# Performance work log

Hardware: AMD Instinct MI355X
Metric: run time of the kernel (lower is better)

## Reference

```python
import jax, jax.numpy as jnp
import numpy as np

DIM = 1024
D_STATE = 16
D_CONV = 4
EXPAND = 2
D_INNER = EXPAND * DIM          # 2048
DT_RANK = (DIM + 15) // 16      # 64 (mamba_ssm 'auto')
B_SZ = 2
SEQ = 1024


def setup_inputs() -> dict:
    key = jax.random.key(0)
    ks = jax.random.split(key, 10)
    s = 0.02
    x = jax.random.normal(ks[0], (B_SZ, SEQ, DIM), jnp.float32)
    mask = jnp.ones((B_SZ, SEQ), dtype=bool)
    in_proj_w = jax.random.normal(ks[1], (DIM, 2 * D_INNER), jnp.float32) * s
    conv_w = jax.random.normal(ks[2], (D_INNER, D_CONV), jnp.float32) * 0.2
    conv_b = jnp.zeros((D_INNER,), jnp.float32)
    x_proj_w = jax.random.normal(ks[3], (D_INNER, DT_RANK + 2 * D_STATE), jnp.float32) * s
    dt_proj_w = jax.random.normal(ks[4], (DT_RANK, D_INNER), jnp.float32) * (DT_RANK ** -0.5)
    # inverse-softplus-style small positive dt bias, like mamba_ssm init
    dt = jnp.exp(jax.random.uniform(ks[5], (D_INNER,)) * (np.log(0.1) - np.log(0.001)) + np.log(0.001))
    dt_proj_b = dt + jnp.log(-jnp.expm1(-dt))
    # A_log init: log(1..d_state) per channel (S4D-real init)
    A_log = jnp.log(jnp.tile(jnp.arange(1, D_STATE + 1, dtype=jnp.float32)[None, :], (D_INNER, 1)))
    D = jnp.ones((D_INNER,), jnp.float32)
    out_proj_w = jax.random.normal(ks[6], (D_INNER, DIM), jnp.float32) * s
    return {"x": x, "mask": mask, "in_proj_w": in_proj_w, "conv_w": conv_w,
            "conv_b": conv_b, "x_proj_w": x_proj_w, "dt_proj_w": dt_proj_w,
            "dt_proj_b": dt_proj_b, "A_log": A_log, "D": D, "out_proj_w": out_proj_w}


def _mamba(x, in_proj_w, conv_w, conv_b, x_proj_w, dt_proj_w, dt_proj_b, A_log, D, out_proj_w):
    B, L, _ = x.shape
    xz = x @ in_proj_w                       # (B, L, 2*d_inner)
    xc, z = jnp.split(xz, 2, axis=-1)
    # causal depthwise conv1d (padding=d_conv-1, truncated to L)
    xp = jnp.pad(xc, ((0, 0), (D_CONV - 1, 0), (0, 0)))
    conv = conv_b
    for k in range(D_CONV):
        conv = conv + xp[:, k:k + L, :] * conv_w[:, k]
    u = jax.nn.silu(conv)                    # (B, L, d_inner)
    x_dbl = u @ x_proj_w                     # (B, L, dt_rank + 2*d_state)
    dtr, Bm, Cm = jnp.split(x_dbl, [DT_RANK, DT_RANK + D_STATE], axis=-1)
    delta = jax.nn.softplus(dtr @ dt_proj_w + dt_proj_b)   # (B, L, d_inner)
    A = -jnp.exp(A_log)                      # (d_inner, d_state)
    dA = jnp.exp(jnp.einsum('bld,dn->bldn', delta, A))     # (B, L, d_inner, d_state)
    dBu = jnp.einsum('bld,bln->bldn', delta * u, Bm)

    def step(h, inp):
        dA_t, dBu_t, C_t = inp
        h = dA_t * h + dBu_t                 # (B, d_inner, d_state)
        y = jnp.einsum('bdn,bn->bd', h, C_t)
        return h, y

    h0 = jnp.zeros((B, D_INNER, D_STATE), x.dtype)
    _, ys = jax.lax.scan(step, h0, (dA.transpose(1, 0, 2, 3),
                                    dBu.transpose(1, 0, 2, 3),
                                    Cm.transpose(1, 0, 2)))
    y = ys.transpose(1, 0, 2) + u * D        # (B, L, d_inner)
    y = y * jax.nn.silu(z)
    return y @ out_proj_w                    # (B, L, dim)


def reference(x, mask, in_proj_w, conv_w, conv_b, x_proj_w, dt_proj_w, dt_proj_b, A_log, D, out_proj_w):
    out = _mamba(x, in_proj_w, conv_w, conv_b, x_proj_w, dt_proj_w, dt_proj_b, A_log, D, out_proj_w)
    # dropout=0.0 -> Identity; masked_fill(~mask, 0)
    return jnp.where(mask[:, :, None], out, 0.0)
```

## Files before the change

kernel.cpp:

```cpp
#include <hip/hip_runtime.h>
#include <hip/hip_bf16.h>

#define DIMX 1024
#define DSTATE 16
#define DCONV 4
#define DINNER 2048
#define DTRANK 64
#define BSZ 2
#define SEQL 1024
#define NROW (BSZ*SEQL)
#define NPROJ (DTRANK + 2*DSTATE)
#define NCH2 32
#define CL2 32
#define G2SPLIT 16
#define G2KLEN (DINNER / G2SPLIT)
#define G4SPLIT 2

typedef __bf16 bf16x8 __attribute__((ext_vector_type(8)));
typedef float f32x4 __attribute__((ext_vector_type(4)));
typedef unsigned short ushort8_t __attribute__((ext_vector_type(8)));

#define LOG2E 1.44269504088896340736f

__device__ __forceinline__ float sigmoidf_(float x){ return 1.0f/(1.0f+__expf(-x)); }
__device__ __forceinline__ float fexp2(float x){ return __builtin_amdgcn_exp2f(x); }
__device__ __forceinline__ unsigned short f2bf(float f){
  union { float f; unsigned int i; } c; c.f = f;
  unsigned int r = (c.i + 0x7FFFu + ((c.i >> 16) & 1u)) >> 16;
  return (unsigned short)r;
}
__device__ __forceinline__ float bf2f(unsigned short u){
  union { unsigned int i; float f; } c; c.i = ((unsigned int)u) << 16; return c.f;
}

__device__ __forceinline__ void gload16(const void* g, void* l){
  __builtin_amdgcn_global_load_lds(
      (const __attribute__((address_space(1))) unsigned int*)g,
      (__attribute__((address_space(3))) unsigned int*)l, 16, 0, 0);
}

__global__ __launch_bounds__(256) void prep_k(
    const float* __restrict__ x, unsigned short* __restrict__ xb,
    const float* __restrict__ w1, unsigned short* __restrict__ w1t,
    const float* __restrict__ w4, unsigned short* __restrict__ w4t,
    const float* __restrict__ dtw, unsigned short* __restrict__ dtwt,
    const float* __restrict__ xpw, unsigned short* __restrict__ xpwt)
{
  __shared__ unsigned short T[32][33];
  int blk = blockIdx.x;
  if (blk < 2048) {
    const int i = blk*256 + threadIdx.x;
    float4 v = *(const float4*)(x + (size_t)i * 4);
    ushort4 o;
    o.x = f2bf(v.x); o.y = f2bf(v.y); o.z = f2bf(v.z); o.w = f2bf(v.w);
    *(ushort4*)(xb + (size_t)i * 4) = o;
    return;
  }
  blk -= 2048;
  if (blk >= 6464) {
    blk -= 6464;
    const int i = blk*256 + threadIdx.x;
    *(ushort4*)(xpwt + (size_t)96*DINNER + (size_t)i*4) = make_ushort4(0,0,0,0);
    return;
  }
  const float* w; unsigned short* wt; int K, N, nT, kT;
  if (blk < 4096) {
    w = w1; wt = w1t; K = 1024; N = 4096;
    nT = (blk & 127) * 32; kT = (blk >> 7) * 32;
  } else if (blk < 6144) {
    blk -= 4096;
    w = w4; wt = w4t; K = 2048; N = 1024;
    nT = (blk & 31) * 32; kT = (blk >> 5) * 32;
  } else if (blk < 6272) {
    blk -= 6144;
    w = dtw; wt = dtwt; K = 64; N = 2048;
    nT = (blk & 63) * 32; kT = (blk >> 6) * 32;
  } else {
    blk -= 6272;
    w = xpw; wt = xpwt; K = 2048; N = 96;
    nT = (blk % 3) * 32; kT = (blk / 3) * 32;
  }
  const int tx = threadIdx.x & 31, ty = threadIdx.x >> 5;
  #pragma unroll
  for (int i = 0; i < 4; i++)
    T[tx][ty + i*8] = f2bf(w[(size_t)(kT + ty + i*8) * N + nT + tx]);
  __syncthreads();
  #pragma unroll
  for (int i = 0; i < 4; i++)
    wt[(size_t)(nT + ty + i*8) * K + kT + tx] = T[ty + i*8][tx];
}

__global__ __launch_bounds__(256) void gemm1_bf2_k(
    const unsigned short* __restrict__ A, int lda,
    const unsigned short* __restrict__ BT, int ldb,
    unsigned short* __restrict__ X0, unsigned short* __restrict__ X1,
    int splitN, int ldc, int K)
{
  constexpr int BM = 128, BN = 128, BK = 32, NB = 4;
  __shared__ unsigned short As[NB][BM*BK];
  __shared__ unsigned short Bs[NB][BN*BK];

  const int tid = threadIdx.x;
  const int w = tid >> 6, lane = tid & 63;
  const int quad = lane >> 4, lrow = lane & 15;
  const int mOff = (w & 1) * 64, nOff = (w >> 1) * 64;
  const int rowTile = blockIdx.y * BM, colTile = blockIdx.x * BN;

  f32x4 acc[4][4] = {};

  const int srow = lane >> 2;
  const int sbyte = (lane & 3) * 16;

  for (int k0 = 0; k0 < K; k0 += NB*BK) {
    #pragma unroll
    for (int hh = 0; hh < NB; hh++) {
      const int kk = k0 + hh*BK;
      const char* aSrc = (const char*)(A  + (size_t)(rowTile + w*32 + srow)*lda + kk) + sbyte;
      const char* bSrc = (const char*)(BT + (size_t)(colTile + w*32 + srow)*ldb + kk) + sbyte;
      gload16(aSrc,                    &As[hh][(w*32     )*32]);
      gload16(aSrc + 16*(size_t)lda*2, &As[hh][(w*32 + 16)*32]);
      gload16(bSrc,                    &Bs[hh][(w*32     )*32]);
      gload16(bSrc + 16*(size_t)ldb*2, &Bs[hh][(w*32 + 16)*32]);
    }
    __syncthreads();

    #pragma unroll
    for (int hh = 0; hh < NB; hh++) {
      bf16x8 af[4], bfr[4];
      #pragma unroll
      for (int mi = 0; mi < 4; mi++)
        af[mi] = *(const bf16x8*)&As[hh][(mOff + mi*16 + lrow)*32 + quad*8];
      #pragma unroll
      for (int ni = 0; ni < 4; ni++)
        bfr[ni] = *(const bf16x8*)&Bs[hh][(nOff + ni*16 + lrow)*32 + quad*8];
      #pragma unroll
      for (int mi = 0; mi < 4; mi++)
        #pragma unroll
        for (int ni = 0; ni < 4; ni++)
          acc[mi][ni] = __builtin_amdgcn_mfma_f32_16x16x32_bf16(
              af[mi], bfr[ni], acc[mi][ni], 0, 0, 0);
    }
    __syncthreads();
  }

  unsigned short* Cb = (colTile < splitN) ? X0 : X1;
  const int cBase = (colTile < splitN) ? colTile : colTile - splitN;

  #pragma unroll
  for (int mi = 0; mi < 4; mi++) {
    #pragma unroll
    for (int ni = 0; ni < 4; ni++) {
      const int row = rowTile + mOff + mi*16 + quad*4;
      const int cc = cBase + nOff + ni*16 + lrow;
      #pragma unroll
      for (int r = 0; r < 4; r++)
        Cb[(size_t)(row + r) * ldc + cc] = f2bf(acc[mi][ni][r]);
    }
  }
}

__global__ __launch_bounds__(256) void gemm2_k(
    const unsigned short* __restrict__ A,
    const unsigned short* __restrict__ BT,
    float* __restrict__ g2p)
{
  constexpr int BM = 64, BK = 32;
  __shared__ unsigned short As[2][BM*BK];
  __shared__ unsigned short Bs[2][128*BK];

  const int tid = threadIdx.x;
  const int w = tid >> 6, lane = tid & 63;
  const int quad = lane >> 4, lrow = lane & 15;
  const int mOff = (w & 1) * 32, nOff = (w >> 1) * 64;
  const int rowTile = blockIdx.x * BM;
  const int kBeg = blockIdx.y * G2KLEN;

  f32x4 acc[2][4] = {};

  const int srow = lane >> 2;
  const int sbyte = (lane & 3) * 16;

  for (int k0 = kBeg; k0 < kBeg + G2KLEN; k0 += 2*BK) {
    #pragma unroll
    for (int hh = 0; hh < 2; hh++) {
      const int kk = k0 + hh*BK;
      const char* aSrc = (const char*)(A  + (size_t)(rowTile + w*16 + srow)*DINNER + kk) + sbyte;
      const char* bSrc = (const char*)(BT + (size_t)(w*32 + srow)*DINNER + kk) + sbyte;
      gload16(aSrc,                       &As[hh][(w*16     )*32]);
      gload16(bSrc,                       &Bs[hh][(w*32     )*32]);
      gload16(bSrc + 16*(size_t)DINNER*2, &Bs[hh][(w*32 + 16)*32]);
    }
    __syncthreads();

    #pragma unroll
    for (int hh = 0; hh < 2; hh++) {
      bf16x8 af[2], bfr[4];
      #pragma unroll
      for (int mi = 0; mi < 2; mi++)
        af[mi] = *(const bf16x8*)&As[hh][(mOff + mi*16 + lrow)*32 + quad*8];
      #pragma unroll
      for (int ni = 0; ni < 4; ni++)
        bfr[ni] = *(const bf16x8*)&Bs[hh][(nOff + ni*16 + lrow)*32 + quad*8];
      #pragma unroll
      for (int mi = 0; mi < 2; mi++)
        #pragma unroll
        for (int ni = 0; ni < 4; ni++)
          acc[mi][ni] = __builtin_amdgcn_mfma_f32_16x16x32_bf16(
              af[mi], bfr[ni], acc[mi][ni], 0, 0, 0);
    }
    __syncthreads();
  }

  float* P = g2p + (size_t)blockIdx.y * NROW * NPROJ;
  #pragma unroll
  for (int mi = 0; mi < 2; mi++) {
    #pragma unroll
    for (int ni = 0; ni < 4; ni++) {
      const int row = rowTile + mOff + mi*16 + quad*4;
      const int col = nOff + ni*16 + lrow;
      if (col >= NPROJ) continue;
      #pragma unroll
      for (int r = 0; r < 4; r++)
        P[(size_t)(row + r) * NPROJ + col] = acc[mi][ni][r];
    }
  }
}

__global__ __launch_bounds__(256) void reduce_xdbl_k(
    const float* __restrict__ g2p, float* __restrict__ xdbl)
{
  const int i = blockIdx.x * 256 + threadIdx.x;
  f32x4 v = *(const f32x4*)(g2p + (size_t)i * 4);
  #pragma unroll
  for (int s = 1; s < G2SPLIT; s++)
    v += *(const f32x4*)(g2p + (size_t)s * NROW * NPROJ + (size_t)i * 4);
  *(f32x4*)(xdbl + (size_t)i * 4) = v;
}

__global__ __launch_bounds__(256) void gemm4_k(
    const unsigned short* __restrict__ A,
    const unsigned short* __restrict__ BT,
    float* __restrict__ g4p)
{
  constexpr int BM = 64, BN = 128, BK = 32, NB = 4;
  constexpr int KCH = DINNER / G4SPLIT;
  __shared__ unsigned short As[NB][BM*BK];
  __shared__ unsigned short Bs[NB][BN*BK];

  const int tid = threadIdx.x;
  const int w = tid >> 6, lane = tid & 63;
  const int quad = lane >> 4, lrow = lane & 15;
  const int mOff = (w & 1) * 32, nOff = (w >> 1) * 64;
  const int rowTile = blockIdx.y * BM, colTile = blockIdx.x * BN;
  const int kBeg = blockIdx.z * KCH;

  f32x4 acc[2][4] = {};

  const int srow = lane >> 2;
  const int sbyte = (lane & 3) * 16;

  for (int k0 = kBeg; k0 < kBeg + KCH; k0 += NB*BK) {
    #pragma unroll
    for (int hh = 0; hh < NB; hh++) {
      const int kk = k0 + hh*BK;
      const char* aSrc = (const char*)(A  + (size_t)(rowTile + w*16 + srow)*DINNER + kk) + sbyte;
      const char* bSrc = (const char*)(BT + (size_t)(colTile + w*32 + srow)*DINNER + kk) + sbyte;
      gload16(aSrc,                       &As[hh][(w*16     )*32]);
      gload16(bSrc,                       &Bs[hh][(w*32     )*32]);
      gload16(bSrc + 16*(size_t)DINNER*2, &Bs[hh][(w*32 + 16)*32]);
    }
    __syncthreads();

    #pragma unroll
    for (int hh = 0; hh < NB; hh++) {
      bf16x8 af[2], bfr[4];
      #pragma unroll
      for (int mi = 0; mi < 2; mi++)
        af[mi] = *(const bf16x8*)&As[hh][(mOff + mi*16 + lrow)*32 + quad*8];
      #pragma unroll
      for (int ni = 0; ni < 4; ni++)
        bfr[ni] = *(const bf16x8*)&Bs[hh][(nOff + ni*16 + lrow)*32 + quad*8];
      #pragma unroll
      for (int mi = 0; mi < 2; mi++)
        #pragma unroll
        for (int ni = 0; ni < 4; ni++)
          acc[mi][ni] = __builtin_amdgcn_mfma_f32_16x16x32_bf16(
              af[mi], bfr[ni], acc[mi][ni], 0, 0, 0);
    }
    __syncthreads();
  }

  float* P = g4p + (size_t)blockIdx.z * NROW * DIMX;
  #pragma unroll
  for (int mi = 0; mi < 2; mi++) {
    #pragma unroll
    for (int ni = 0; ni < 4; ni++) {
      const int row = rowTile + mOff + mi*16 + quad*4;
      const int col = colTile + nOff + ni*16 + lrow;
      #pragma unroll
      for (int r = 0; r < 4; r++)
        P[(size_t)(row + r) * DIMX + col] = acc[mi][ni][r];
    }
  }
}

__global__ __launch_bounds__(256) void reduce_out_k(
    const float* __restrict__ g4p, float* __restrict__ outp)
{
  const int i = blockIdx.x * 256 + threadIdx.x;
  f32x4 v = *(const f32x4*)(g4p + (size_t)i * 4);
  #pragma unroll
  for (int s = 1; s < G4SPLIT; s++)
    v += *(const f32x4*)(g4p + (size_t)s * NROW * DIMX + (size_t)i * 4);
  *(f32x4*)(outp + (size_t)i * 4) = v;
}

__global__ __launch_bounds__(256) void gemm3_k(
    const float* __restrict__ xdbl,
    const unsigned short* __restrict__ dtwt,
    const float* __restrict__ bias,
    unsigned short* __restrict__ delta16)
{
  __shared__ float As[64][68];
  __shared__ float Bs[64][68];
  const int tid = threadIdx.x;
  const int tx = tid & 15, ty = tid >> 4;
  const int rowTile = blockIdx.y * 64;
  const int colTile = blockIdx.x * 64;

  const int ar = tid >> 2;
  const int ak = (tid & 3) * 4;

  #pragma unroll
  for (int kc = 0; kc < 4; kc++) {
    const int kk = kc*16 + ak;
    float4 av = *(const float4*)(xdbl + (size_t)(rowTile + ar) * NPROJ + kk);
    As[kk+0][ar] = av.x; As[kk+1][ar] = av.y;
    As[kk+2][ar] = av.z; As[kk+3][ar] = av.w;
    ushort4 bv = *(const ushort4*)(dtwt + (size_t)(colTile + ar) * DTRANK + kk);
    Bs[kk+0][ar] = bf2f(bv.x); Bs[kk+1][ar] = bf2f(bv.y);
    Bs[kk+2][ar] = bf2f(bv.z); Bs[kk+3][ar] = bf2f(bv.w);
  }
  __syncthreads();

  float acc[4][4] = {};
  #pragma unroll 8
  for (int k = 0; k < DTRANK; k++) {
    float4 a4 = *(const float4*)&As[k][ty*4];
    float4 b4 = *(const float4*)&Bs[k][tx*4];
    float a[4] = {a4.x, a4.y, a4.z, a4.w};
    float b[4] = {b4.x, b4.y, b4.z, b4.w};
    #pragma unroll
    for (int i = 0; i < 4; i++)
      #pragma unroll
      for (int j = 0; j < 4; j++)
        acc[i][j] += a[i] * b[j];
  }

  float4 bb = *(const float4*)(bias + colTile + tx*4);
  const float bvv[4] = {bb.x, bb.y, bb.z, bb.w};
  #pragma unroll
  for (int i = 0; i < 4; i++) {
    const int r = rowTile + ty*4 + i;
    ushort4 o;
    float vv[4];
    #pragma unroll
    for (int j = 0; j < 4; j++) {
      float v = acc[i][j] + bvv[j];
      vv[j] = (v > 20.f) ? v : log1pf(__expf(v));
    }
    o.x = f2bf(vv[0]); o.y = f2bf(vv[1]); o.z = f2bf(vv[2]); o.w = f2bf(vv[3]);
    *(ushort4*)(delta16 + (size_t)r * DINNER + colTile + tx*4) = o;
  }
}

__global__ __launch_bounds__(256) void conv_silu_k(
    const unsigned short* __restrict__ xcb,
    const float* __restrict__ conv_w,
    const float* __restrict__ conv_b,
    unsigned short* __restrict__ ub)
{
  const int idx = blockIdx.x * 256 + threadIdx.x;
  const int d4 = (idx & (DINNER/4 - 1)) * 4;
  const int row = idx >> 9;
  const int l = row & (SEQL - 1);

  float4 cb = *(const float4*)(conv_b + d4);
  float acc[4] = {cb.x, cb.y, cb.z, cb.w};
  float4 w0 = *(const float4*)(conv_w + (size_t)(d4+0)*4);
  float4 w1 = *(const float4*)(conv_w + (size_t)(d4+1)*4);
  float4 w2 = *(const float4*)(conv_w + (size_t)(d4+2)*4);
  float4 w3 = *(const float4*)(conv_w + (size_t)(d4+3)*4);
  const float* wp[4] = {(const float*)&w0, (const float*)&w1,
                        (const float*)&w2, (const float*)&w3};
  #pragma unroll
  for (int k = 0; k < DCONV; k++) {
    const int ls = l + k - (DCONV - 1);
    if (ls >= 0) {
      ushort4 xv = *(const ushort4*)(xcb + (size_t)(row + k - (DCONV - 1)) * DINNER + d4);
      acc[0] += bf2f(xv.x) * wp[0][k];
      acc[1] += bf2f(xv.y) * wp[1][k];
      acc[2] += bf2f(xv.z) * wp[2][k];
      acc[3] += bf2f(xv.w) * wp[3][k];
    }
  }
  ushort4 o;
  o.x = f2bf(acc[0] * sigmoidf_(acc[0]));
  o.y = f2bf(acc[1] * sigmoidf_(acc[1]));
  o.z = f2bf(acc[2] * sigmoidf_(acc[2]));
  o.w = f2bf(acc[3] * sigmoidf_(acc[3]));
  *(ushort4*)(ub + (size_t)row * DINNER + d4) = o;
}

__global__ __launch_bounds__(256) void scan_a(
    const unsigned short* __restrict__ delta16,
    const unsigned short* __restrict__ ub,
    const float* __restrict__ xdbl,
    const float* __restrict__ A_log,
    float* __restrict__ S, float* __restrict__ sumd_g)
{
  const int bx = blockIdx.x;
  const int c  = bx & (NCH2-1);
  const int dg = (bx / NCH2) & 7;
  const int b  = bx / (NCH2*8);
  const int d = dg * 256 + threadIdx.x;
  const size_t row0 = (size_t)(b*SEQL + c*CL2);

  __shared__ float bc_s[CL2][32];
  {
    const int t = threadIdx.x >> 3;
    const int cc = (threadIdx.x & 7) * 4;
    *(float4*)&bc_s[t][cc] = *(const float4*)&xdbl[(row0 + t)*NPROJ + DTRANK + cc];
  }

  float A2[16];
  #pragma unroll
  for (int i = 0; i < 4; i++) {
    float4 al = *(const float4*)&A_log[(size_t)d*DSTATE + i*4];
    A2[i*4+0] = -__expf(al.x)*LOG2E; A2[i*4+1] = -__expf(al.y)*LOG2E;
    A2[i*4+2] = -__expf(al.z)*LOG2E; A2[i*4+3] = -__expf(al.w)*LOG2E;
  }

  float dlt[CL2], uu[CL2];
  #pragma unroll
  for (int t = 0; t < CL2; t++) {
    dlt[t] = bf2f(delta16[(row0 + t)*DINNER + d]);
    uu[t]  = bf2f(ub[(row0 + t)*DINNER + d]);
  }
  __syncthreads();

  float h[16];
  #pragma unroll
  for (int n = 0; n < 16; n++) h[n] = 0.f;
  float sd = 0.f;

  #pragma unroll
  for (int t = 0; t < CL2; t++) {
    const float du = dlt[t] * uu[t];
    sd += dlt[t];
    f32x4 bq[4];
    #pragma unroll
    for (int i = 0; i < 4; i++) bq[i] = *(const f32x4*)&bc_s[t][i*4];
    #pragma unroll
    for (int n = 0; n < 16; n++) {
      const float a = fexp2(dlt[t] * A2[n]);
      h[n] = a * h[n] + du * bq[n>>2][n&3];
    }
  }

  const size_t base = ((size_t)(b*NCH2 + c) * DINNER + d) * DSTATE;
  #pragma unroll
  for (int i = 0; i < 4; i++) {
    f32x4 hv; hv[0]=h[i*4+0]; hv[1]=h[i*4+1]; hv[2]=h[i*4+2]; hv[3]=h[i*4+3];
    *(f32x4*)&S[base + i*4] = hv;
  }
  sumd_g[(size_t)(b*NCH2 + c) * DINNER + d] = sd;
}

__global__ __launch_bounds__(256) void scan_b(
    const float* __restrict__ S, const float* __restrict__ sumd_g,
    const float* __restrict__ A_log, float* __restrict__ H)
{
  const int idx = blockIdx.x * 256 + threadIdx.x;
  const int n = idx & 15, d = (idx >> 4) & (DINNER-1), b = idx >> 15;
  const float A2 = -__expf(A_log[(size_t)d*DSTATE + n]) * LOG2E;
  float h = 0.f;
  size_t pos = ((size_t)(b*NCH2) * DINNER + d) * DSTATE + n;
  size_t sp  = (size_t)(b*NCH2) * DINNER + d;
  const size_t pstep = (size_t)DINNER * DSTATE;
  #pragma unroll 4
  for (int c = 0; c < NCH2; c++) {
    const float sd = sumd_g[sp];
    const float Sv = S[pos];
    H[pos] = h;
    h = fexp2(A2 * sd) * h + Sv;
    pos += pstep; sp += DINNER;
  }
}

__global__ __launch_bounds__(256) void scan_c(
    const unsigned short* __restrict__ delta16,
    const unsigned short* __restrict__ ub,
    const unsigned short* __restrict__ zb,
    const float* __restrict__ xdbl,
    const float* __restrict__ A_log,
    const float* __restrict__ Dp,
    const float* __restrict__ H,
    unsigned short* __restrict__ Y)
{
  const int bx = blockIdx.x;
  const int c  = bx & (NCH2-1);
  const int dg = (bx / NCH2) & 7;
  const int b  = bx / (NCH2*8);
  const int d = dg * 256 + threadIdx.x;
  const size_t row0 = (size_t)(b*SEQL + c*CL2);

  __shared__ float bc_s[CL2][32];
  {
    const int t = threadIdx.x >> 3;
    const int cc = (threadIdx.x & 7) * 4;
    *(float4*)&bc_s[t][cc] = *(const float4*)&xdbl[(row0 + t)*NPROJ + DTRANK + cc];
  }

  float A2[16];
  #pragma unroll
  for (int i = 0; i < 4; i++) {
    float4 al = *(const float4*)&A_log[(size_t)d*DSTATE + i*4];
    A2[i*4+0] = -__expf(al.x)*LOG2E; A2[i*4+1] = -__expf(al.y)*LOG2E;
    A2[i*4+2] = -__expf(al.z)*LOG2E; A2[i*4+3] = -__expf(al.w)*LOG2E;
  }
  const float Dval = Dp[d];

  float dlt[CL2], uu[CL2], zz[CL2];
  #pragma unroll
  for (int t = 0; t < CL2; t++) {
    dlt[t] = bf2f(delta16[(row0 + t)*DINNER + d]);
    uu[t]  = bf2f(ub[(row0 + t)*DINNER + d]);
    zz[t]  = bf2f(zb[(row0 + t)*DINNER + d]);
  }

  float h[16];
  {
    const size_t hb = ((size_t)(b*NCH2 + c) * DINNER + d) * DSTATE;
    #pragma unroll
    for (int i = 0; i < 4; i++) {
      f32x4 hv = *(const f32x4*)&H[hb + i*4];
      h[i*4+0]=hv[0]; h[i*4+1]=hv[1]; h[i*4+2]=hv[2]; h[i*4+3]=hv[3];
    }
  }
  __syncthreads();

  #pragma unroll
  for (int t = 0; t < CL2; t++) {
    const float du = dlt[t] * uu[t];
    f32x4 bq[4], cq[4];
    #pragma unroll
    for (int i = 0; i < 4; i++) {
      bq[i] = *(const f32x4*)&bc_s[t][i*4];
      cq[i] = *(const f32x4*)&bc_s[t][16 + i*4];
    }
    float y = 0.f;
    #pragma unroll
    for (int n = 0; n < 16; n++) {
      const float a = fexp2(dlt[t] * A2[n]);
      h[n] = a * h[n] + du * bq[n>>2][n&3];
      y += h[n] * cq[n>>2][n&3];
    }
    const float yy = (y + uu[t]*Dval) * (zz[t] * sigmoidf_(zz[t]));
    Y[(row0 + t)*DINNER + d] = f2bf(yy);
  }
}

extern "C" void kernel_launch(void* const* d_in, const int* in_sizes, int n_in,
                              void* d_out, int out_size, void* d_ws, size_t ws_size,
                              hipStream_t stream) {
  const float* x         = (const float*)d_in[0];
  const float* in_proj_w = (const float*)d_in[2];
  const float* conv_w    = (const float*)d_in[3];
  const float* conv_b    = (const float*)d_in[4];
  const float* x_proj_w  = (const float*)d_in[5];
  const float* dt_proj_w = (const float*)d_in[6];
  const float* dt_proj_b = (const float*)d_in[7];
  const float* A_log     = (const float*)d_in[8];
  const float* Dp        = (const float*)d_in[9];
  const float* out_proj_w= (const float*)d_in[10];
  float* out = (float*)d_out;

  char* B = (char*)d_ws;
  unsigned short* xcb  = (unsigned short*)B;
  unsigned short* yb   = (unsigned short*)B;
  float* xdbl = (float*)(B + (34ll<<20));
  unsigned short* delta16 = (unsigned short*)(B + (35ll<<20));
  unsigned short* w1t  = (unsigned short*)(B + (44ll<<20));
  unsigned short* w4t  = (unsigned short*)(B + (53ll<<20));
  unsigned short* dtwt = (unsigned short*)(B + (58ll<<20));
  unsigned short* xb   = (unsigned short*)(B + (59ll<<20));
  unsigned short* xpwt = (unsigned short*)(B + (64ll<<20));
  float* S2   = (float*)(B + (72ll<<20));
  float* H2   = (float*)(B + (90ll<<20));
  float* sumd = (float*)(B + (108ll<<20));
  unsigned short* zb = (unsigned short*)(B + (110ll<<20));
  unsigned short* ub = (unsigned short*)(B + (119ll<<20));
  float* g4p  = (float*)(B + (136ll<<20));
  float* g2p  = (float*)(B + (172ll<<20));

  dim3 blk(256);

  prep_k<<<dim3(2048 + 4096 + 2048 + 128 + 192 + 64), blk, 0, stream>>>(
      x, xb, in_proj_w, w1t, out_proj_w, w4t, dt_proj_w, dtwt, x_proj_w, xpwt);

  gemm1_bf2_k<<<dim3((2*DINNER)/128, NROW/128), blk, 0, stream>>>(
      xb, DIMX, w1t, DIMX, xcb, zb, DINNER, DINNER, DIMX);

  conv_silu_k<<<(NROW*DINNER/4)/256, blk, 0, stream>>>(xcb, conv_w, conv_b, ub);

  gemm2_k<<<dim3(NROW/64, G2SPLIT), blk, 0, stream>>>(ub, xpwt, g2p);
  reduce_xdbl_k<<<(NROW*NPROJ/4)/256, blk, 0, stream>>>(g2p, xdbl);

  gemm3_k<<<dim3(DINNER/64, NROW/64), blk, 0, stream>>>(
      xdbl, dtwt, dt_proj_b, delta16);

  scan_a<<<dim3(BSZ*NCH2*8), blk, 0, stream>>>(delta16, ub, xdbl, A_log, S2, sumd);
  scan_b<<<dim3((BSZ*DINNER*DSTATE)/256), blk, 0, stream>>>(S2, sumd, A_log, H2);
  scan_c<<<dim3(BSZ*NCH2*8), blk, 0, stream>>>(
      delta16, ub, zb, xdbl, A_log, Dp, H2, yb);

  gemm4_k<<<dim3(DIMX/128, NROW/64, G4SPLIT), blk, 0, stream>>>(yb, w4t, g4p);
  reduce_out_k<<<(NROW*DIMX/4)/256, blk, 0, stream>>>(g4p, out);
}
```

Before: 228.9 us.

## Double-buffer LDS tiles in in_proj and out_proj GEMMs to overlap loads with MFMA

Both the in_proj GEMM and the split-K out_proj GEMM now use two shared-memory buffers, each holding half the previous K depth. The next K-chunk's global-to-LDS loads are issued right after the barrier, before the MFMA work on the current buffer. This hides global load latency behind compute and removes one barrier per iteration. Total LDS use stays the same, but each stage is shallower, so the loop runs twice as many iterations.

```diff
diff --git a/kernel.cpp b/kernel.cpp
--- a/kernel.cpp
+++ b/kernel.cpp
@@ -96,9 +96,9 @@
     unsigned short* __restrict__ X0, unsigned short* __restrict__ X1,
     int splitN, int ldc, int K)
 {
-  constexpr int BM = 128, BN = 128, BK = 32, NB = 4;
-  __shared__ unsigned short As[NB][BM*BK];
-  __shared__ unsigned short Bs[NB][BN*BK];
+  constexpr int BM = 128, BN = 128, BK = 32, NB = 2;
+  __shared__ unsigned short As[2][NB][BM*BK];
+  __shared__ unsigned short Bs[2][NB][BN*BK];
 
   const int tid = threadIdx.x;
   const int w = tid >> 6, lane = tid & 63;
@@ -111,28 +111,33 @@
   const int srow = lane >> 2;
   const int sbyte = (lane & 3) * 16;
 
+  const char* aBase = (const char*)(A  + (size_t)(rowTile + w*32 + srow)*lda) + sbyte;
+  const char* bBase = (const char*)(BT + (size_t)(colTile + w*32 + srow)*ldb) + sbyte;
+
+  #define G1_STAGE(buf, k0)                                              \
+    _Pragma("unroll")                                                    \
+    for (int hh = 0; hh < NB; hh++) {                                    \
+      const int kk = (k0) + hh*BK;                                       \
+      gload16(aBase + (size_t)kk*2,                 &As[buf][hh][(w*32     )*32]); \
+      gload16(aBase + (size_t)kk*2 + 16*(size_t)lda*2, &As[buf][hh][(w*32 + 16)*32]); \
+      gload16(bBase + (size_t)kk*2,                 &Bs[buf][hh][(w*32     )*32]); \
+      gload16(bBase + (size_t)kk*2 + 16*(size_t)ldb*2, &Bs[buf][hh][(w*32 + 16)*32]); \
+    }
+
+  G1_STAGE(0, 0);
+  int cur = 0;
   for (int k0 = 0; k0 < K; k0 += NB*BK) {
-    #pragma unroll
-    for (int hh = 0; hh < NB; hh++) {
-      const int kk = k0 + hh*BK;
-      const char* aSrc = (const char*)(A  + (size_t)(rowTile + w*32 + srow)*lda + kk) + sbyte;
-      const char* bSrc = (const char*)(BT + (size_t)(colTile + w*32 + srow)*ldb + kk) + sbyte;
-      gload16(aSrc,                    &As[hh][(w*32     )*32]);
-      gload16(aSrc + 16*(size_t)lda*2, &As[hh][(w*32 + 16)*32]);
-      gload16(bSrc,                    &Bs[hh][(w*32     )*32]);
-      gload16(bSrc + 16*(size_t)ldb*2, &Bs[hh][(w*32 + 16)*32]);
-    }
     __syncthreads();
-
+    if (k0 + NB*BK < K) { G1_STAGE(cur ^ 1, k0 + NB*BK); }
     #pragma unroll
     for (int hh = 0; hh < NB; hh++) {
       bf16x8 af[4], bfr[4];
       #pragma unroll
       for (int mi = 0; mi < 4; mi++)
-        af[mi] = *(const bf16x8*)&As[hh][(mOff + mi*16 + lrow)*32 + quad*8];
+        af[mi] = *(const bf16x8*)&As[cur][hh][(mOff + mi*16 + lrow)*32 + quad*8];
       #pragma unroll
       for (int ni = 0; ni < 4; ni++)
-        bfr[ni] = *(const bf16x8*)&Bs[hh][(nOff + ni*16 + lrow)*32 + quad*8];
+        bfr[ni] = *(const bf16x8*)&Bs[cur][hh][(nOff + ni*16 + lrow)*32 + quad*8];
       #pragma unroll
       for (int mi = 0; mi < 4; mi++)
         #pragma unroll
@@ -140,8 +145,9 @@
           acc[mi][ni] = __builtin_amdgcn_mfma_f32_16x16x32_bf16(
               af[mi], bfr[ni], acc[mi][ni], 0, 0, 0);
     }
-    __syncthreads();
-  }
+    cur ^= 1;
+  }
+  #undef G1_STAGE
 
   unsigned short* Cb = (colTile < splitN) ? X0 : X1;
   const int cBase = (colTile < splitN) ? colTile : colTile - splitN;
@@ -242,10 +248,10 @@
     const unsigned short* __restrict__ BT,
     float* __restrict__ g4p)
 {
-  constexpr int BM = 64, BN = 128, BK = 32, NB = 4;
+  constexpr int BM = 64, BN = 128, BK = 32, NB = 2;
   constexpr int KCH = DINNER / G4SPLIT;
-  __shared__ unsigned short As[NB][BM*BK];
-  __shared__ unsigned short Bs[NB][BN*BK];
+  __shared__ unsigned short As[2][NB][BM*BK];
+  __shared__ unsigned short Bs[2][NB][BN*BK];
 
   const int tid = threadIdx.x;
   const int w = tid >> 6, lane = tid & 63;
@@ -259,27 +265,32 @@
   const int srow = lane >> 2;
   const int sbyte = (lane & 3) * 16;
 
+  const char* aBase = (const char*)(A  + (size_t)(rowTile + w*16 + srow)*DINNER) + sbyte;
+  const char* bBase = (const char*)(BT + (size_t)(colTile + w*32 + srow)*DINNER) + sbyte;
+
+  #define G4_STAGE(buf, k0)                                              \
+    _Pragma("unroll")                                                    \
+    for (int hh = 0; hh < NB; hh++) {                                    \
+      const int kk = (k0) + hh*BK;                                       \
+      gload16(aBase + (size_t)kk*2,                    &As[buf][hh][(w*16     )*32]); \
+      gload16(bBase + (size_t)kk*2,                    &Bs[buf][hh][(w*32     )*32]); \
+      gload16(bBase + (size_t)kk*2 + 16*(size_t)DINNER*2, &Bs[buf][hh][(w*32 + 16)*32]); \
+    }
+
+  G4_STAGE(0, kBeg);
+  int cur = 0;
   for (int k0 = kBeg; k0 < kBeg + KCH; k0 += NB*BK) {
-    #pragma unroll
-    for (int hh = 0; hh < NB; hh++) {
-      const int kk = k0 + hh*BK;
-      const char* aSrc = (const char*)(A  + (size_t)(rowTile + w*16 + srow)*DINNER + kk) + sbyte;
-      const char* bSrc = (const char*)(BT + (size_t)(colTile + w*32 + srow)*DINNER + kk) + sbyte;
-      gload16(aSrc,                       &As[hh][(w*16     )*32]);
-      gload16(bSrc,                       &Bs[hh][(w*32     )*32]);
-      gload16(bSrc + 16*(size_t)DINNER*2, &Bs[hh][(w*32 + 16)*32]);
-    }
     __syncthreads();
-
+    if (k0 + NB*BK < kBeg + KCH) { G4_STAGE(cur ^ 1, k0 + NB*BK); }
     #pragma unroll
     for (int hh = 0; hh < NB; hh++) {
       bf16x8 af[2], bfr[4];
       #pragma unroll
       for (int mi = 0; mi < 2; mi++)
-        af[mi] = *(const bf16x8*)&As[hh][(mOff + mi*16 + lrow)*32 + quad*8];
+        af[mi] = *(const bf16x8*)&As[cur][hh][(mOff + mi*16 + lrow)*32 + quad*8];
       #pragma unroll
       for (int ni = 0; ni < 4; ni++)
-        bfr[ni] = *(const bf16x8*)&Bs[hh][(nOff + ni*16 + lrow)*32 + quad*8];
+        bfr[ni] = *(const bf16x8*)&Bs[cur][hh][(nOff + ni*16 + lrow)*32 + quad*8];
       #pragma unroll
       for (int mi = 0; mi < 2; mi++)
         #pragma unroll
@@ -287,8 +298,9 @@
           acc[mi][ni] = __builtin_amdgcn_mfma_f32_16x16x32_bf16(
               af[mi], bfr[ni], acc[mi][ni], 0, 0, 0);
     }
-    __syncthreads();
-  }
+    cur ^= 1;
+  }
+  #undef G4_STAGE
 
   float* P = g4p + (size_t)blockIdx.z * NROW * DIMX;
   #pragma unroll
```

After: 235.9 us. 3.1% more time.
